# Performance work log

Hardware: AMD Instinct MI355X
Metric: run time of the kernel (lower is better)

## Reference

```python
import jax, jax.numpy as jnp
import numpy as np

# Grid / model dims
B, H, W = 1, 90, 180
P = H * W                 # 16200 spatial points
MODEL_DIM = 130
L = MODEL_DIM - 2         # learnable_dim = 128
NH, HD = 8, 16            # n_heads, head_dim
S = 16                    # shared_hidden (DISCO out_channels)
K = 25                    # number of DISCO basis functions (piecewise-linear 5x5)
NNB = 25                  # neighbors per output point (theta_cutoff stencil)
MH = 32                   # head MLP hidden
FH = 256                  # FFN hidden


def setup_inputs() -> dict:
    key = jax.random.key(0)
    ks = jax.random.split(key, 12)
    x = jax.random.normal(ks[0], (B, H, W, MODEL_DIM), dtype=jnp.float32)
    # sparse DISCO structure: neighbor indices + precomputed (quadrature-weighted) basis values
    nbr_idx = jax.random.randint(ks[1], (P, NNB), 0, P, dtype=jnp.int32)
    basis_vals = jax.random.normal(ks[2], (K, P, NNB), dtype=jnp.float32) * 0.1
    # learnable DISCO kernel weights (out_channels=S, in_channels=1, K basis coeffs) + bias
    disco_w = jax.random.normal(ks[3], (S, K), dtype=jnp.float32) / np.sqrt(K).astype(np.float32)
    disco_b = jax.random.normal(ks[4], (S,), dtype=jnp.float32) * 0.01
    # per-head MLP params: S -> MH -> 1, one set per head
    head_w1 = jax.random.normal(ks[5], (NH, S, MH), dtype=jnp.float32) / np.sqrt(S).astype(np.float32)
    head_b1 = jnp.zeros((NH, MH), dtype=jnp.float32)
    head_w2 = jax.random.normal(ks[6], (NH, MH, 1), dtype=jnp.float32) / np.sqrt(MH).astype(np.float32)
    head_b2 = jnp.zeros((NH, 1), dtype=jnp.float32)
    # FFN: model_dim -> FH -> L, with the sin/cos input columns zeroed (as in __init__)
    ffn_w1 = jax.random.normal(ks[7], (MODEL_DIM, FH), dtype=jnp.float32) / np.sqrt(MODEL_DIM).astype(np.float32)
    ffn_w1 = ffn_w1.at[-2:, :].set(0.0)
    ffn_b1 = jnp.zeros((FH,), dtype=jnp.float32)
    ffn_w2 = jax.random.normal(ks[8], (FH, L), dtype=jnp.float32) / np.sqrt(FH).astype(np.float32)
    ffn_b2 = jnp.zeros((L,), dtype=jnp.float32)
    return dict(x=x, nbr_idx=nbr_idx, basis_vals=basis_vals, disco_w=disco_w, disco_b=disco_b,
                head_w1=head_w1, head_b1=head_b1, head_w2=head_w2, head_b2=head_b2,
                ffn_w1=ffn_w1, ffn_b1=ffn_b1, ffn_w2=ffn_w2, ffn_b2=ffn_b2)


def reference(x, nbr_idx, basis_vals, disco_w, disco_b,
              head_w1, head_b1, head_w2, head_b2,
              ffn_w1, ffn_b1, ffn_w2, ffn_b2):
    gelu = lambda t: jax.nn.gelu(t, approximate=False)  # torch nn.GELU default is exact
    x_learn = x[..., :L]          # (B,H,W,L)
    sin_cos = x[..., L:]          # (B,H,W,2)
    x_res = x_learn

    # ---- DISCO spherical conv, depthwise over B*L channels (in_channels=1) ----
    xf = jnp.transpose(x_learn, (0, 3, 1, 2)).reshape(B * L, P)      # (N, P)
    gathered = xf[:, nbr_idx]                                        # (N, P, NNB) irregular gather
    z = jnp.einsum('kpn,cpn->ckp', basis_vals, gathered)             # (N, K, P) basis projections
    y = jnp.einsum('sk,ckp->csp', disco_w, z) + disco_b[None, :, None]  # (N, S, P)
    disco_out = y.reshape(B, L, S, H, W).transpose(0, 3, 4, 1, 2)    # (B,H,W,L,S)

    # ---- per-head MLP, vectorized over heads ----
    hfeat = disco_out.reshape(B, H, W, NH, HD, S)                    # (B,H,W,NH,HD,S)
    h1 = gelu(jnp.einsum('bxyhds,hsm->bxyhdm', hfeat, head_w1) + head_b1[:, None, :])
    hout = jnp.einsum('bxyhdm,hmo->bxyhdo', h1, head_w2) + head_b2[:, None, :]  # o=1
    x_mix = hout.reshape(B, H, W, L)                                 # heads concatenated in order
    x_mix = x_mix + x_res                                            # residual

    # ---- FFN channel mixing on [x_mix, sin_cos] ----
    x_full = jnp.concatenate([x_mix, sin_cos], axis=-1)              # (B,H,W,MODEL_DIM)
    hf = gelu(jnp.einsum('bxyd,df->bxyf', x_full, ffn_w1) + ffn_b1)
    x_ffn = jnp.einsum('bxyf,fl->bxyl', hf, ffn_w2) + ffn_b2
    x_out = x_ffn + x_mix
    return jnp.concatenate([x_out, sin_cos], axis=-1)                # (B,H,W,MODEL_DIM)
```

## Files before the change

### kernel.cpp

```cpp
#include <hip/hip_runtime.h>
#include <hip/hip_bf16.h>

#define P_TOT 16200
#define MODEL_DIMC 130
#define L_DIM 128
#define NHH 8
#define HDD 16
#define S_DIM 16
#define K_DIM 25
#define NNBC 25
#define MH_DIM 32
#define FH_DIM 256

__device__ __forceinline__ float gelu_f(float x) {
    float z = fabsf(x) * 0.70710678118654752440f;
    float t = __builtin_amdgcn_rcpf(fmaf(0.3275911f, z, 1.0f));
    float poly = t * fmaf(t, fmaf(t, fmaf(t, fmaf(t, 1.061405429f, -1.453152027f),
                                          1.421413741f), -0.284496736f), 0.254829592f);
    float e = __expf(-z * z);
    float erfp = fmaf(-poly, e, 1.0f);
    float erfv = copysignf(erfp, x);
    return 0.5f * x * (1.0f + erfv);
}

__global__ __launch_bounds__(256) void k1_bw(const float* __restrict__ basis,
                                             const float* __restrict__ disco_w,
                                             float* __restrict__ bw) {
    __shared__ float w[S_DIM * K_DIM];
    int tid = threadIdx.x;
    for (int i = tid; i < S_DIM * K_DIM; i += 256) w[i] = disco_w[i];
    __syncthreads();
    int i = blockIdx.x * 256 + tid;
    if (i >= P_TOT * NNBC) return;
    float bv[K_DIM];
#pragma unroll
    for (int k = 0; k < K_DIM; k++) bv[k] = basis[k * (P_TOT * NNBC) + i];
    float acc[S_DIM];
#pragma unroll
    for (int s = 0; s < S_DIM; s++) {
        float a = 0.f;
#pragma unroll
        for (int k = 0; k < K_DIM; k++) a = fmaf(w[s * K_DIM + k], bv[k], a);
        acc[s] = a;
    }
    float4* outp = (float4*)(bw + (size_t)i * S_DIM);
#pragma unroll
    for (int q = 0; q < 4; q++) {
        float4 v; v.x = acc[q*4+0]; v.y = acc[q*4+1]; v.z = acc[q*4+2]; v.w = acc[q*4+3];
        outp[q] = v;
    }
}

__global__ __launch_bounds__(256) void k2_disco_head(
        const float* __restrict__ x, const int* __restrict__ nbr,
        const float* __restrict__ bw,
        const float* __restrict__ head_w1, const float* __restrict__ head_b1,
        const float* __restrict__ head_w2, const float* __restrict__ head_b2,
        const float* __restrict__ disco_b,
        float* __restrict__ xmix) {
    __shared__ __align__(16) float w1t[NHH * 516];
    __shared__ float b1s[NHH * 33];
    __shared__ float w2s[NHH * 33];
    __shared__ float b2s[NHH];
    __shared__ float dbs[S_DIM];
    __shared__ __align__(16) float bws[2][NNBC * S_DIM];
    __shared__ int nbrs[2][NNBC];

    int tid = threadIdx.x;
    for (int i = tid; i < NHH * S_DIM * MH_DIM; i += 256) {
        int h = i >> 9, s = (i >> 5) & 15, m = i & 31;
        w1t[h * 516 + m * 16 + s] = head_w1[i];
    }
    for (int i = tid; i < NHH * MH_DIM; i += 256) {
        int h = i >> 5, m = i & 31;
        b1s[h * 33 + m] = head_b1[i];
        w2s[h * 33 + m] = head_w2[i];
    }
    if (tid < NHH) b2s[tid] = head_b2[tid];
    if (tid < S_DIM) dbs[tid] = disco_b[tid];

    int p0 = blockIdx.x * 2;
    {
        const float4* src = (const float4*)(bw + (size_t)p0 * (NNBC * S_DIM));
        float4* dst = (float4*)&bws[0][0];
        for (int j = tid; j < (2 * NNBC * S_DIM) / 4; j += 256) dst[j] = src[j];
    }
    if (tid < 2 * NNBC) nbrs[0][tid] = nbr[p0 * NNBC + tid];
    __syncthreads();

    int wv = tid >> 6, lane = tid & 63;
    int ptl = wv >> 1;
    int c = (wv & 1) * 64 + lane;
    int p = p0 + ptl;

    float y[16];
#pragma unroll
    for (int s = 0; s < 16; s++) y[s] = dbs[s];

    const float* xb = x + c;
#pragma unroll 5
    for (int nb = 0; nb < NNBC; nb += 5) {
        float g[5];
#pragma unroll
        for (int j = 0; j < 5; j++) {
            int u = nbrs[ptl][nb + j];
            g[j] = xb[(size_t)u * MODEL_DIMC];
        }
#pragma unroll
        for (int j = 0; j < 5; j++) {
            const float4* bwn = (const float4*)&bws[ptl][(nb + j) * 16];
#pragma unroll
            for (int q = 0; q < 4; q++) {
                float4 b4 = bwn[q];
                y[q*4+0] = fmaf(g[j], b4.x, y[q*4+0]);
                y[q*4+1] = fmaf(g[j], b4.y, y[q*4+1]);
                y[q*4+2] = fmaf(g[j], b4.z, y[q*4+2]);
                y[q*4+3] = fmaf(g[j], b4.w, y[q*4+3]);
            }
        }
    }

    int h = c >> 4;
    float acc = b2s[h];
    const float* wrow = &w1t[h * 516];
    const float* b1r  = &b1s[h * 33];
    const float* w2r  = &w2s[h * 33];
#pragma unroll 4
    for (int m = 0; m < MH_DIM; m++) {
        float a = b1r[m];
        const float4* r = (const float4*)&wrow[m * 16];
#pragma unroll
        for (int q = 0; q < 4; q++) {
            float4 wa = r[q];
            a = fmaf(y[q*4+0], wa.x, a);
            a = fmaf(y[q*4+1], wa.y, a);
            a = fmaf(y[q*4+2], wa.z, a);
            a = fmaf(y[q*4+3], wa.w, a);
        }
        a = gelu_f(a);
        acc = fmaf(a, w2r[m], acc);
    }
    xmix[p * L_DIM + c] = acc + x[(size_t)p * MODEL_DIMC + c];
}

__global__ __launch_bounds__(256) void k3_ffn(
        const float* __restrict__ x, const float* __restrict__ xmix,
        const float* __restrict__ w1, const float* __restrict__ b1,
        const float* __restrict__ w2, const float* __restrict__ b2,
        float* __restrict__ out) {
    __shared__ __align__(16) float xm[32 * 128];
    __shared__ __align__(16) float hf[32 * 260];
    int tid = threadIdx.x;
    int p0 = blockIdx.x * 32;
    int valid = min(32, P_TOT - p0);
    {
        int nf4 = (valid * 128) / 4;
        const float4* src = (const float4*)(xmix + (size_t)p0 * 128);
        float4* dst = (float4*)xm;
        for (int j = tid; j < nf4; j += 256) dst[j] = src[j];
    }
    __syncthreads();

    int fg = tid & 31, pg = tid >> 5;
    float acc[4][8];
#pragma unroll
    for (int i = 0; i < 4; i++)
#pragma unroll
        for (int j = 0; j < 8; j++) acc[i][j] = b1[fg * 8 + j];

#pragma unroll 4
    for (int k = 0; k < 128; k++) {
        float4 wA = *(const float4*)&w1[k * FH_DIM + fg * 8];
        float4 wB = *(const float4*)&w1[k * FH_DIM + fg * 8 + 4];
#pragma unroll
        for (int i = 0; i < 4; i++) {
            float xv = xm[(pg * 4 + i) * 128 + k];
            acc[i][0] = fmaf(xv, wA.x, acc[i][0]);
            acc[i][1] = fmaf(xv, wA.y, acc[i][1]);
            acc[i][2] = fmaf(xv, wA.z, acc[i][2]);
            acc[i][3] = fmaf(xv, wA.w, acc[i][3]);
            acc[i][4] = fmaf(xv, wB.x, acc[i][4]);
            acc[i][5] = fmaf(xv, wB.y, acc[i][5]);
            acc[i][6] = fmaf(xv, wB.z, acc[i][6]);
            acc[i][7] = fmaf(xv, wB.w, acc[i][7]);
        }
    }
#pragma unroll
    for (int i = 0; i < 4; i++) {
        int pl = pg * 4 + i;
#pragma unroll
        for (int j = 0; j < 8; j++) hf[pl * 260 + fg * 8 + j] = gelu_f(acc[i][j]);
    }
    __syncthreads();

    int lg = tid & 31;
    float acc2[4][4];
#pragma unroll
    for (int i = 0; i < 4; i++)
#pragma unroll
        for (int j = 0; j < 4; j++) acc2[i][j] = b2[lg * 4 + j];

#pragma unroll 4
    for (int f = 0; f < FH_DIM; f++) {
        float4 wv = *(const float4*)&w2[f * L_DIM + lg * 4];
#pragma unroll
        for (int i = 0; i < 4; i++) {
            float hv = hf[(pg * 4 + i) * 260 + f];
            acc2[i][0] = fmaf(hv, wv.x, acc2[i][0]);
            acc2[i][1] = fmaf(hv, wv.y, acc2[i][1]);
            acc2[i][2] = fmaf(hv, wv.z, acc2[i][2]);
            acc2[i][3] = fmaf(hv, wv.w, acc2[i][3]);
        }
    }
#pragma unroll
    for (int i = 0; i < 4; i++) {
        int pl = pg * 4 + i;
        if (pl < valid) {
            int p = p0 + pl;
            float2 o01, o23;
            o01.x = acc2[i][0] + xm[pl * 128 + lg * 4 + 0];
            o01.y = acc2[i][1] + xm[pl * 128 + lg * 4 + 1];
            o23.x = acc2[i][2] + xm[pl * 128 + lg * 4 + 2];
            o23.y = acc2[i][3] + xm[pl * 128 + lg * 4 + 3];
            *(float2*)&out[p * MODEL_DIMC + lg * 4 + 0] = o01;
            *(float2*)&out[p * MODEL_DIMC + lg * 4 + 2] = o23;
            if (lg == 0) {
                float2 sc;
                sc.x = x[p * MODEL_DIMC + 128];
                sc.y = x[p * MODEL_DIMC + 129];
                *(float2*)&out[p * MODEL_DIMC + 128] = sc;
            }
        }
    }
}

extern "C" void kernel_launch(void* const* d_in, const int* in_sizes, int n_in,
                              void* d_out, int out_size, void* d_ws, size_t ws_size,
                              hipStream_t stream) {
    const float* x        = (const float*)d_in[0];
    const int*   nbr      = (const int*)  d_in[1];
    const float* basis    = (const float*)d_in[2];
    const float* disco_w  = (const float*)d_in[3];
    const float* disco_b  = (const float*)d_in[4];
    const float* head_w1  = (const float*)d_in[5];
    const float* head_b1  = (const float*)d_in[6];
    const float* head_w2  = (const float*)d_in[7];
    const float* head_b2  = (const float*)d_in[8];
    const float* ffn_w1   = (const float*)d_in[9];
    const float* ffn_b1   = (const float*)d_in[10];
    const float* ffn_w2   = (const float*)d_in[11];
    const float* ffn_b2   = (const float*)d_in[12];
    float* out = (float*)d_out;

    float* bw   = (float*)d_ws;
    float* xmix = bw + (size_t)P_TOT * NNBC * S_DIM;

    hipLaunchKernelGGL(k1_bw, dim3((P_TOT * NNBC + 255) / 256), dim3(256), 0, stream,
                       basis, disco_w, bw);
    hipLaunchKernelGGL(k2_disco_head, dim3(P_TOT / 2), dim3(256), 0, stream,
                       x, nbr, bw, head_w1, head_b1, head_w2, head_b2, disco_b, xmix);
    hipLaunchKernelGGL(k3_ffn, dim3((P_TOT + 31) / 32), dim3(256), 0, stream,
                       x, xmix, ffn_w1, ffn_b1, ffn_w2, ffn_b2, out);
}
```

Measured before the change: 259.7 us.

## Restructure DISCO head kernel per-wave and split FFN into two kernels

The head weight transpose moves into a separate tiny kernel, so the DISCO kernel no longer rebuilds large shared tables in every block. Each wave now owns one point and covers all 128 channels, reading basis weights and neighbor indices straight from global memory as uniform loads. The y features are regrouped through LDS so each lane computes one head channel for four points. The FFN is split into two kernels with hidden activations staged in global workspace, reusing the bw buffer. This lowers per-block setup and register/LDS pressure at the cost of an extra launch and a global round trip of the hidden activations.

```diff
diff --git a/kernel.cpp b/kernel.cpp
--- a/kernel.cpp
+++ b/kernel.cpp
@@ -5,7 +5,6 @@
 #define MODEL_DIMC 130
 #define L_DIM 128
 #define NHH 8
-#define HDD 16
 #define S_DIM 16
 #define K_DIM 25
 #define NNBC 25
@@ -21,6 +20,15 @@
     float erfp = fmaf(-poly, e, 1.0f);
     float erfv = copysignf(erfp, x);
     return 0.5f * x * (1.0f + erfv);
+}
+
+__global__ __launch_bounds__(256) void k0_transpose_w1(const float* __restrict__ hw1,
+                                                       float* __restrict__ w1t) {
+    int i = blockIdx.x * 256 + threadIdx.x;
+    if (i < NHH * S_DIM * MH_DIM) {
+        int h = i >> 9, s = (i >> 5) & 15, m = i & 31;
+        w1t[h * 512 + m * 16 + s] = hw1[i];
+    }
 }
 
 __global__ __launch_bounds__(256) void k1_bw(const float* __restrict__ basis,
@@ -51,185 +59,209 @@
     }
 }
 
-__global__ __launch_bounds__(256) void k2_disco_head(
+#define YSTR 2056
+__global__ __launch_bounds__(256, 4) void k2_disco_head(
         const float* __restrict__ x, const int* __restrict__ nbr,
-        const float* __restrict__ bw,
-        const float* __restrict__ head_w1, const float* __restrict__ head_b1,
-        const float* __restrict__ head_w2, const float* __restrict__ head_b2,
-        const float* __restrict__ disco_b,
+        const float* __restrict__ bw, const float* __restrict__ w1t,
+        const float* __restrict__ head_b1, const float* __restrict__ head_w2,
+        const float* __restrict__ head_b2, const float* __restrict__ disco_b,
         float* __restrict__ xmix) {
-    __shared__ __align__(16) float w1t[NHH * 516];
-    __shared__ float b1s[NHH * 33];
-    __shared__ float w2s[NHH * 33];
-    __shared__ float b2s[NHH];
-    __shared__ float dbs[S_DIM];
-    __shared__ __align__(16) float bws[2][NNBC * S_DIM];
-    __shared__ int nbrs[2][NNBC];
-
-    int tid = threadIdx.x;
-    for (int i = tid; i < NHH * S_DIM * MH_DIM; i += 256) {
-        int h = i >> 9, s = (i >> 5) & 15, m = i & 31;
-        w1t[h * 516 + m * 16 + s] = head_w1[i];
-    }
-    for (int i = tid; i < NHH * MH_DIM; i += 256) {
-        int h = i >> 5, m = i & 31;
-        b1s[h * 33 + m] = head_b1[i];
-        w2s[h * 33 + m] = head_w2[i];
-    }
-    if (tid < NHH) b2s[tid] = head_b2[tid];
-    if (tid < S_DIM) dbs[tid] = disco_b[tid];
-
-    int p0 = blockIdx.x * 2;
+    __shared__ float ylds[4 * YSTR];
+
+    int tid  = threadIdx.x;
+    int lane = tid & 63;
+    int wv   = __builtin_amdgcn_readfirstlane(tid >> 6);
+    int p0   = blockIdx.x * 4;
+    int p    = p0 + wv;
+
+    const float* bwp = bw + (size_t)p * (NNBC * S_DIM);
+    const int*   nbp = nbr + p * NNBC;
+
+    float y0[16], y1[16];
+#pragma unroll
+    for (int s = 0; s < 16; s++) { float db = disco_b[s]; y0[s] = db; y1[s] = db; }
+
+    const float* xb0 = x + lane;
+    const float* xb1 = x + 64 + lane;
+
+#pragma unroll 1
+    for (int nb = 0; nb < 24; nb += 4) {
+#pragma unroll
+        for (int j = 0; j < 4; j++) {
+            int u = nbp[nb + j];
+            float g0 = xb0[(size_t)u * MODEL_DIMC];
+            float g1 = xb1[(size_t)u * MODEL_DIMC];
+#pragma unroll
+            for (int s = 0; s < 16; s++) {
+                float wv_ = bwp[(nb + j) * 16 + s];
+                y0[s] = fmaf(g0, wv_, y0[s]);
+                y1[s] = fmaf(g1, wv_, y1[s]);
+            }
+        }
+    }
     {
-        const float4* src = (const float4*)(bw + (size_t)p0 * (NNBC * S_DIM));
-        float4* dst = (float4*)&bws[0][0];
-        for (int j = tid; j < (2 * NNBC * S_DIM) / 4; j += 256) dst[j] = src[j];
-    }
-    if (tid < 2 * NNBC) nbrs[0][tid] = nbr[p0 * NNBC + tid];
+        int u = nbp[24];
+        float g0 = xb0[(size_t)u * MODEL_DIMC];
+        float g1 = xb1[(size_t)u * MODEL_DIMC];
+#pragma unroll
+        for (int s = 0; s < 16; s++) {
+            float wv_ = bwp[24 * 16 + s];
+            y0[s] = fmaf(g0, wv_, y0[s]);
+            y1[s] = fmaf(g1, wv_, y1[s]);
+        }
+    }
+
+#pragma unroll
+    for (int s = 0; s < 16; s++) {
+        ylds[wv * YSTR + s * 128 + lane]      = y0[s];
+        ylds[wv * YSTR + s * 128 + 64 + lane] = y1[s];
+    }
     __syncthreads();
 
-    int wv = tid >> 6, lane = tid & 63;
-    int ptl = wv >> 1;
-    int c = (wv & 1) * 64 + lane;
-    int p = p0 + ptl;
-
-    float y[16];
-#pragma unroll
-    for (int s = 0; s < 16; s++) y[s] = dbs[s];
-
-    const float* xb = x + c;
-#pragma unroll 5
-    for (int nb = 0; nb < NNBC; nb += 5) {
-        float g[5];
-#pragma unroll
-        for (int j = 0; j < 5; j++) {
-            int u = nbrs[ptl][nb + j];
-            g[j] = xb[(size_t)u * MODEL_DIMC];
-        }
-#pragma unroll
-        for (int j = 0; j < 5; j++) {
-            const float4* bwn = (const float4*)&bws[ptl][(nb + j) * 16];
-#pragma unroll
-            for (int q = 0; q < 4; q++) {
-                float4 b4 = bwn[q];
-                y[q*4+0] = fmaf(g[j], b4.x, y[q*4+0]);
-                y[q*4+1] = fmaf(g[j], b4.y, y[q*4+1]);
-                y[q*4+2] = fmaf(g[j], b4.z, y[q*4+2]);
-                y[q*4+3] = fmaf(g[j], b4.w, y[q*4+3]);
-            }
-        }
-    }
-
-    int h = c >> 4;
-    float acc = b2s[h];
-    const float* wrow = &w1t[h * 516];
-    const float* b1r  = &b1s[h * 33];
-    const float* w2r  = &w2s[h * 33];
-#pragma unroll 4
-    for (int m = 0; m < MH_DIM; m++) {
-        float a = b1r[m];
-        const float4* r = (const float4*)&wrow[m * 16];
-#pragma unroll
-        for (int q = 0; q < 4; q++) {
-            float4 wa = r[q];
-            a = fmaf(y[q*4+0], wa.x, a);
-            a = fmaf(y[q*4+1], wa.y, a);
-            a = fmaf(y[q*4+2], wa.z, a);
-            a = fmaf(y[q*4+3], wa.w, a);
-        }
-        a = gelu_f(a);
-        acc = fmaf(a, w2r[m], acc);
-    }
-    xmix[p * L_DIM + c] = acc + x[(size_t)p * MODEL_DIMC + c];
-}
-
-__global__ __launch_bounds__(256) void k3_ffn(
-        const float* __restrict__ x, const float* __restrict__ xmix,
-        const float* __restrict__ w1, const float* __restrict__ b1,
-        const float* __restrict__ w2, const float* __restrict__ b2,
-        float* __restrict__ out) {
-    __shared__ __align__(16) float xm[32 * 128];
-    __shared__ __align__(16) float hf[32 * 260];
+    int ptl = lane >> 4;
+    int d   = lane & 15;
+#pragma unroll
+    for (int t = 0; t < 2; t++) {
+        int hh = __builtin_amdgcn_readfirstlane(wv + 4 * t);
+        float yv[16];
+#pragma unroll
+        for (int s = 0; s < 16; s++)
+            yv[s] = ylds[ptl * YSTR + s * 128 + hh * 16 + d];
+        const float* wrow = w1t + hh * (MH_DIM * S_DIM);
+        const float* b1r  = head_b1 + hh * MH_DIM;
+        const float* w2r  = head_w2 + hh * MH_DIM;
+        float acc = head_b2[hh];
+#pragma unroll 2
+        for (int m = 0; m < MH_DIM; m++) {
+            float a = b1r[m];
+#pragma unroll
+            for (int s = 0; s < 16; s++)
+                a = fmaf(yv[s], wrow[m * 16 + s], a);
+            a = gelu_f(a);
+            acc = fmaf(a, w2r[m], acc);
+        }
+        int pp = p0 + ptl;
+        int c  = hh * 16 + d;
+        xmix[pp * L_DIM + c] = acc + x[(size_t)pp * MODEL_DIMC + c];
+    }
+}
+
+__global__ __launch_bounds__(256, 4) void k3a_ffn1(
+        const float* __restrict__ xmix, const float* __restrict__ w1,
+        const float* __restrict__ b1, float* __restrict__ hf) {
+    __shared__ __align__(16) float xm[32 * 132];
     int tid = threadIdx.x;
     int p0 = blockIdx.x * 32;
     int valid = min(32, P_TOT - p0);
     {
-        int nf4 = (valid * 128) / 4;
-        const float4* src = (const float4*)(xmix + (size_t)p0 * 128);
-        float4* dst = (float4*)xm;
-        for (int j = tid; j < nf4; j += 256) dst[j] = src[j];
+        const float4* src = (const float4*)(xmix + (size_t)p0 * L_DIM);
+        for (int j = tid; j < valid * 32; j += 256) {
+            float4 v = src[j];
+            int pt = j >> 5, q = j & 31;
+            *(float4*)&xm[pt * 132 + q * 4] = v;
+        }
     }
     __syncthreads();
 
-    int fg = tid & 31, pg = tid >> 5;
-    float acc[4][8];
-#pragma unroll
-    for (int i = 0; i < 4; i++)
-#pragma unroll
-        for (int j = 0; j < 8; j++) acc[i][j] = b1[fg * 8 + j];
-
-#pragma unroll 4
+    int fg = tid & 15, pg = tid >> 4;
+    int f0 = fg * 16;
+    float acc[2][16];
+#pragma unroll
+    for (int j = 0; j < 16; j++) { float bb = b1[f0 + j]; acc[0][j] = bb; acc[1][j] = bb; }
+    const float* xr0 = &xm[(pg * 2 + 0) * 132];
+    const float* xr1 = &xm[(pg * 2 + 1) * 132];
+#pragma unroll 2
     for (int k = 0; k < 128; k++) {
-        float4 wA = *(const float4*)&w1[k * FH_DIM + fg * 8];
-        float4 wB = *(const float4*)&w1[k * FH_DIM + fg * 8 + 4];
+        float xa = xr0[k], xb = xr1[k];
+        const float4* wr = (const float4*)&w1[k * FH_DIM + f0];
+#pragma unroll
+        for (int q = 0; q < 4; q++) {
+            float4 w4 = wr[q];
+            acc[0][q*4+0] = fmaf(xa, w4.x, acc[0][q*4+0]);
+            acc[0][q*4+1] = fmaf(xa, w4.y, acc[0][q*4+1]);
+            acc[0][q*4+2] = fmaf(xa, w4.z, acc[0][q*4+2]);
+            acc[0][q*4+3] = fmaf(xa, w4.w, acc[0][q*4+3]);
+            acc[1][q*4+0] = fmaf(xb, w4.x, acc[1][q*4+0]);
+            acc[1][q*4+1] = fmaf(xb, w4.y, acc[1][q*4+1]);
+            acc[1][q*4+2] = fmaf(xb, w4.z, acc[1][q*4+2]);
+            acc[1][q*4+3] = fmaf(xb, w4.w, acc[1][q*4+3]);
+        }
+    }
+#pragma unroll
+    for (int i = 0; i < 2; i++) {
+        int pl = pg * 2 + i;
+        if (pl < valid) {
+            float4* hp = (float4*)(hf + (size_t)(p0 + pl) * FH_DIM + f0);
+#pragma unroll
+            for (int q = 0; q < 4; q++) {
+                float4 v;
+                v.x = gelu_f(acc[i][q*4+0]);
+                v.y = gelu_f(acc[i][q*4+1]);
+                v.z = gelu_f(acc[i][q*4+2]);
+                v.w = gelu_f(acc[i][q*4+3]);
+                hp[q] = v;
+            }
+        }
+    }
+}
+
+__global__ __launch_bounds__(256, 4) void k3b_ffn2(
+        const float* __restrict__ x, const float* __restrict__ xmix,
+        const float* __restrict__ hf, const float* __restrict__ w2,
+        const float* __restrict__ b2, float* __restrict__ out) {
+    __shared__ __align__(16) float hfl[32 * 260];
+    int tid = threadIdx.x;
+    int p0 = blockIdx.x * 32;
+    int valid = min(32, P_TOT - p0);
+    {
+        const float4* src = (const float4*)(hf + (size_t)p0 * FH_DIM);
+        for (int j = tid; j < valid * 64; j += 256) {
+            float4 v = src[j];
+            int pt = j >> 6, q = j & 63;
+            *(float4*)&hfl[pt * 260 + q * 4] = v;
+        }
+    }
+    __syncthreads();
+
+    int lg = tid & 31, pg = tid >> 5;
+    float4 bb = *(const float4*)&b2[lg * 4];
+    float acc2[4][4];
+#pragma unroll
+    for (int i = 0; i < 4; i++) {
+        acc2[i][0] = bb.x; acc2[i][1] = bb.y; acc2[i][2] = bb.z; acc2[i][3] = bb.w;
+    }
+#pragma unroll 2
+    for (int f = 0; f < FH_DIM; f++) {
+        float4 wv4 = *(const float4*)&w2[f * L_DIM + lg * 4];
 #pragma unroll
         for (int i = 0; i < 4; i++) {
-            float xv = xm[(pg * 4 + i) * 128 + k];
-            acc[i][0] = fmaf(xv, wA.x, acc[i][0]);
-            acc[i][1] = fmaf(xv, wA.y, acc[i][1]);
-            acc[i][2] = fmaf(xv, wA.z, acc[i][2]);
-            acc[i][3] = fmaf(xv, wA.w, acc[i][3]);
-            acc[i][4] = fmaf(xv, wB.x, acc[i][4]);
-            acc[i][5] = fmaf(xv, wB.y, acc[i][5]);
-            acc[i][6] = fmaf(xv, wB.z, acc[i][6]);
-            acc[i][7] = fmaf(xv, wB.w, acc[i][7]);
-        }
-    }
-#pragma unroll
-    for (int i = 0; i < 4; i++) {
-        int pl = pg * 4 + i;
-#pragma unroll
-        for (int j = 0; j < 8; j++) hf[pl * 260 + fg * 8 + j] = gelu_f(acc[i][j]);
-    }
-    __syncthreads();
-
-    int lg = tid & 31;
-    float acc2[4][4];
-#pragma unroll
-    for (int i = 0; i < 4; i++)
-#pragma unroll
-        for (int j = 0; j < 4; j++) acc2[i][j] = b2[lg * 4 + j];
-
-#pragma unroll 4
-    for (int f = 0; f < FH_DIM; f++) {
-        float4 wv = *(const float4*)&w2[f * L_DIM + lg * 4];
-#pragma unroll
-        for (int i = 0; i < 4; i++) {
-            float hv = hf[(pg * 4 + i) * 260 + f];
-            acc2[i][0] = fmaf(hv, wv.x, acc2[i][0]);
-            acc2[i][1] = fmaf(hv, wv.y, acc2[i][1]);
-            acc2[i][2] = fmaf(hv, wv.z, acc2[i][2]);
-            acc2[i][3] = fmaf(hv, wv.w, acc2[i][3]);
+            float hv = hfl[(pg * 4 + i) * 260 + f];
+            acc2[i][0] = fmaf(hv, wv4.x, acc2[i][0]);
+            acc2[i][1] = fmaf(hv, wv4.y, acc2[i][1]);
+            acc2[i][2] = fmaf(hv, wv4.z, acc2[i][2]);
+            acc2[i][3] = fmaf(hv, wv4.w, acc2[i][3]);
         }
     }
 #pragma unroll
     for (int i = 0; i < 4; i++) {
         int pl = pg * 4 + i;
         if (pl < valid) {
-            int p = p0 + pl;
+            int pp = p0 + pl;
+            float4 xm4 = *(const float4*)&xmix[(size_t)pp * L_DIM + lg * 4];
             float2 o01, o23;
-            o01.x = acc2[i][0] + xm[pl * 128 + lg * 4 + 0];
-            o01.y = acc2[i][1] + xm[pl * 128 + lg * 4 + 1];
-            o23.x = acc2[i][2] + xm[pl * 128 + lg * 4 + 2];
-            o23.y = acc2[i][3] + xm[pl * 128 + lg * 4 + 3];
-            *(float2*)&out[p * MODEL_DIMC + lg * 4 + 0] = o01;
-            *(float2*)&out[p * MODEL_DIMC + lg * 4 + 2] = o23;
-            if (lg == 0) {
-                float2 sc;
-                sc.x = x[p * MODEL_DIMC + 128];
-                sc.y = x[p * MODEL_DIMC + 129];
-                *(float2*)&out[p * MODEL_DIMC + 128] = sc;
-            }
+            o01.x = acc2[i][0] + xm4.x;
+            o01.y = acc2[i][1] + xm4.y;
+            o23.x = acc2[i][2] + xm4.z;
+            o23.y = acc2[i][3] + xm4.w;
+            *(float2*)&out[(size_t)pp * MODEL_DIMC + lg * 4]     = o01;
+            *(float2*)&out[(size_t)pp * MODEL_DIMC + lg * 4 + 2] = o23;
+        }
+    }
+    if (tid < 64) {
+        int pt = tid >> 1, wch = tid & 1;
+        if (pt < valid) {
+            int pp = p0 + pt;
+            out[(size_t)pp * MODEL_DIMC + 128 + wch] = x[(size_t)pp * MODEL_DIMC + 128 + wch];
         }
     }
 }
@@ -254,11 +286,16 @@
 
     float* bw   = (float*)d_ws;
     float* xmix = bw + (size_t)P_TOT * NNBC * S_DIM;
-
+    float* w1t  = xmix + (size_t)P_TOT * L_DIM;
+    float* hf   = bw;
+
+    hipLaunchKernelGGL(k0_transpose_w1, dim3(16), dim3(256), 0, stream, head_w1, w1t);
     hipLaunchKernelGGL(k1_bw, dim3((P_TOT * NNBC + 255) / 256), dim3(256), 0, stream,
                        basis, disco_w, bw);
-    hipLaunchKernelGGL(k2_disco_head, dim3(P_TOT / 2), dim3(256), 0, stream,
-                       x, nbr, bw, head_w1, head_b1, head_w2, head_b2, disco_b, xmix);
-    hipLaunchKernelGGL(k3_ffn, dim3((P_TOT + 31) / 32), dim3(256), 0, stream,
-                       x, xmix, ffn_w1, ffn_b1, ffn_w2, ffn_b2, out);
-}
+    hipLaunchKernelGGL(k2_disco_head, dim3(P_TOT / 4), dim3(256), 0, stream,
+                       x, nbr, bw, w1t, head_b1, head_w2, head_b2, disco_b, xmix);
+    hipLaunchKernelGGL(k3a_ffn1, dim3((P_TOT + 31) / 32), dim3(256), 0, stream,
+                       xmix, ffn_w1, ffn_b1, hf);
+    hipLaunchKernelGGL(k3b_ffn2, dim3((P_TOT + 31) / 32), dim3(256), 0, stream,
+                       x, xmix, hf, ffn_w2, ffn_b2, out);
+}
```

Result: slower. 323.0 us (+24.4%).
